# Kernel tuning notes

Measured on AMD Instinct MI355X. Metric: run time of the kernel, lower is better.

## Reference

```python
import jax, jax.numpy as jnp
import numpy as np

H = W = 512
P = H * W          # total superpixel member pixels
N_SP = 1024        # number of superpixels


def _conv(x, w, b):
    # x: [N,C,H,W], w: [O,I,3,3] -> [N,O,H,W], SAME padding
    y = jax.lax.conv_general_dilated(
        x, w, window_strides=(1, 1), padding='SAME',
        dimension_numbers=('NCHW', 'OIHW', 'NCHW'))
    return y + b[None, :, None, None]


def _embed(raw, w1, b1, w2, b2, w3, b3):
    h = jax.nn.relu(_conv(raw, w1, b1))
    h = jax.nn.relu(_conv(h, w2, b2))
    return _conv(h, w3, b3)  # [1, 10, H, W]


def setup_inputs() -> dict:
    key = jax.random.key(0)
    ks = jax.random.split(key, 6)
    raw = jax.random.normal(ks[0], (1, 1, H, W), dtype=jnp.float32)
    w1 = jax.random.normal(ks[1], (64, 1, 3, 3), dtype=jnp.float32) * 0.3
    b1 = jnp.zeros((64,), jnp.float32)
    w2 = jax.random.normal(ks[2], (64, 64, 3, 3), dtype=jnp.float32) * 0.05
    b2 = jnp.zeros((64,), jnp.float32)
    w3 = jax.random.normal(ks[3], (10, 64, 3, 3), dtype=jnp.float32) * 0.05
    b3 = jnp.zeros((10,), jnp.float32)
    pix_rc = jax.random.randint(ks[4], (P, 2), 0, H, dtype=jnp.int32)
    seg_ids = jax.random.randint(ks[5], (P,), 0, N_SP, dtype=jnp.int32)
    return {"raw": raw, "w1": w1, "b1": b1, "w2": w2, "b2": b2,
            "w3": w3, "b3": b3, "pix_rc": pix_rc, "seg_ids": seg_ids,
            "n_sp": N_SP}


def reference(raw, w1, b1, w2, b2, w3, b3, pix_rc, seg_ids, n_sp):
    feats = _embed(raw, w1, b1, w2, b2, w3, b3)  # [1, C, H, W]
    f = feats[0]                                  # [C, H, W]
    # gather per-pixel feature vectors: [P, C]
    vals = f[:, pix_rc[:, 0], pix_rc[:, 1]].T
    # scatter-mean over superpixels (= per-sp sum / mass)
    sums = jax.ops.segment_sum(vals, seg_ids, num_segments=n_sp)      # [n_sp, C]
    cnts = jax.ops.segment_sum(jnp.ones((vals.shape[0],), vals.dtype),
                               seg_ids, num_segments=n_sp)            # [n_sp]
    return sums / jnp.maximum(cnts, 1.0)[:, None]
```

## Files before the change

### kernel.cpp

```cpp
#include <hip/hip_runtime.h>

typedef __attribute__((ext_vector_type(8))) short short8;
typedef __attribute__((ext_vector_type(4))) float f32x4;

constexpr int H = 512, W = 512;
constexpr int P = H * W;
constexpr int NSP = 1024;
constexpr int SBLK = 512;
constexpr int FGRP = 16;

__device__ inline unsigned short f2bf(float f) {
  unsigned u = __builtin_bit_cast(unsigned, f);
  unsigned r = (u + 0x7fffu + ((u >> 16) & 1u)) >> 16;
  return (unsigned short)r;
}
__device__ inline float bflo(unsigned u) { return __builtin_bit_cast(float, u << 16); }
__device__ inline float bfhi(unsigned u) { return __builtin_bit_cast(float, u & 0xffff0000u); }

__device__ inline int xcd_swz(int b, int cpx) { return (b & 7) * cpx + (b >> 3); }

__global__ __launch_bounds__(256) void prep_k(const float* __restrict__ w2,
                                              const float* __restrict__ w3,
                                              unsigned short* __restrict__ wt2s,
                                              unsigned short* __restrict__ wt3s,
                                              unsigned short* __restrict__ zeros) {
  if (blockIdx.x == 0 && threadIdx.x < 128) zeros[threadIdx.x] = 0;
  int i = blockIdx.x * 256 + threadIdx.x;
  if (i < 36864) {
    int k = i >> 11;
    int t = (i >> 3) & 255;
    int e = i & 7;
    int r = t >> 2, sp = t & 3, s = sp ^ (r & 3);
    int tap = k >> 1, ic = (k & 1) * 32 + s * 8 + e;
    wt2s[i] = f2bf(w2[r * 576 + ic * 9 + tap]);
  } else if (i < 46080) {
    int j = i - 36864;
    int k = j >> 9;
    int t = (j >> 3) & 63;
    int e = j & 7;
    int r = t >> 2, sp = t & 3, s = sp ^ (r & 3);
    int tap = k >> 1, ic = (k & 1) * 32 + s * 8 + e;
    wt3s[j] = (r < 10) ? f2bf(w3[r * 576 + ic * 9 + tap]) : (unsigned short)0;
  }
}

__global__ __launch_bounds__(512) void conv2_k(const float* __restrict__ raw,
                                               const float* __restrict__ w1,
                                               const float* __restrict__ b1,
                                               const unsigned short* __restrict__ wts,
                                               const float* __restrict__ bias,
                                               unsigned short* __restrict__ ynhwc) {
  constexpr int WCS = 2048;
  __shared__ __align__(16) unsigned short acts[352 * 64];
  __shared__ __align__(16) unsigned short wbuf[3 * WCS];
  __shared__ float rawt[12 * 36];
  int tid = threadIdx.x;
  int lane = tid & 63, wave = tid >> 6;
  int logical = xcd_swz(blockIdx.x, 128);
  int tilex = logical & 15, tiley = logical >> 4;
  int c0 = tilex * 32, r0 = tiley * 8;

  if (tid < 256) {
#pragma unroll
    for (int k0 = 0; k0 < 2; ++k0) {
      const unsigned short* src = wts + (size_t)k0 * WCS + tid * 8;
      unsigned short* dstb = wbuf + k0 * WCS + wave * 512;
      __builtin_amdgcn_global_load_lds((const __attribute__((address_space(1))) void*)src,
                                       (__attribute__((address_space(3))) void*)dstb, 16, 0, 0);
    }
  }
  if (tid < 432) {
    int rr = tid / 36, cc = tid - rr * 36;
    int gr = r0 + rr - 2, gc = c0 + cc - 2;
    bool ok = ((unsigned)gr < 512u) && ((unsigned)gc < 512u);
    rawt[tid] = ok ? raw[gr * 512 + gc] : 0.f;
  }

  int q = lane >> 4, n = lane & 15;
  int og1 = wave & 3;
  short8 a1f;
  {
    short av[8];
#pragma unroll
    for (int e = 0; e < 8; ++e) av[e] = 0;
    int oc = og1 * 16 + n;
    if (q == 0) {
#pragma unroll
      for (int e = 0; e < 8; ++e) av[e] = (short)f2bf(w1[oc * 9 + e]);
    } else if (q == 1) {
      av[0] = (short)f2bf(w1[oc * 9 + 8]);
    }
    a1f = (short8){av[0], av[1], av[2], av[3], av[4], av[5], av[6], av[7]};
  }
  float bb1[4];
#pragma unroll
  for (int r2 = 0; r2 < 4; ++r2) bb1[r2] = b1[og1 * 16 + q * 4 + r2];
  __syncthreads();

  char* actw = (char*)acts;
  int tbase = (wave < 4) ? 0 : 11;
  for (int ti = 0; ti < 11; ++ti) {
    int t = tbase + ti;
    int px = t * 16 + n;
    bool okp = px < 340;
    int prow = px / 34, pcol = px - prow * 34;
    int prc = okp ? prow : 9;
    short bv[8];
#pragma unroll
    for (int e = 0; e < 8; ++e) bv[e] = 0;
    if (q == 0) {
#pragma unroll
      for (int e = 0; e < 8; ++e) {
        int dy = e / 3, dx = e - dy * 3;
        bv[e] = (short)f2bf(rawt[(prc + dy) * 36 + pcol + dx]);
      }
    } else if (q == 1) {
      bv[0] = (short)f2bf(rawt[(prc + 2) * 36 + pcol + 2]);
    }
    short8 b1f = (short8){bv[0], bv[1], bv[2], bv[3], bv[4], bv[5], bv[6], bv[7]};
    f32x4 d = __builtin_amdgcn_mfma_f32_16x16x32_bf16(a1f, b1f,
                                                       (f32x4){0.f, 0.f, 0.f, 0.f}, 0, 0, 0);
    int gr1 = r0 + prow - 1, gc1 = c0 + pcol - 1;
    bool ok1 = okp && ((unsigned)gr1 < 512u) && ((unsigned)gc1 < 512u);
    float o0 = ok1 ? fmaxf(d.x + bb1[0], 0.f) : 0.f;
    float o1 = ok1 ? fmaxf(d.y + bb1[1], 0.f) : 0.f;
    float o2 = ok1 ? fmaxf(d.z + bb1[2], 0.f) : 0.f;
    float o3 = ok1 ? fmaxf(d.w + bb1[3], 0.f) : 0.f;
    unsigned lo = (unsigned)f2bf(o0) | ((unsigned)f2bf(o1) << 16);
    unsigned hi = (unsigned)f2bf(o2) | ((unsigned)f2bf(o3) << 16);
    int wa = px * 128 + ((((og1 * 2 + (q >> 1)) ^ (px & 7)) << 4)) + ((q & 1) << 3);
    *reinterpret_cast<uint2*>(actw + wa) = make_uint2(lo, hi);
  }
  __syncthreads();

  f32x4 acc[4][2];
#pragma unroll
  for (int og = 0; og < 4; ++og)
#pragma unroll
    for (int g = 0; g < 2; ++g) acc[og][g] = (f32x4){0.f, 0.f, 0.f, 0.f};

  int plbase[2];
#pragma unroll
  for (int g = 0; g < 2; ++g) plbase[g] = wave * 34 + 16 * g + n;
  const char* actb = (const char*)acts;

#pragma unroll
  for (int k = 0; k < 18; ++k) {
    if (k == 17) {
      asm volatile("s_waitcnt vmcnt(0)" ::: "memory");
    } else {
      asm volatile("s_waitcnt vmcnt(1)" ::: "memory");
    }
    __builtin_amdgcn_sched_barrier(0);
    __builtin_amdgcn_s_barrier();
    __builtin_amdgcn_sched_barrier(0);
    if (k + 2 < 18 && tid < 256) {
      const unsigned short* src = wts + (size_t)(k + 2) * WCS + tid * 8;
      unsigned short* dstb = wbuf + ((k + 2) % 3) * WCS + wave * 512;
      __builtin_amdgcn_global_load_lds((const __attribute__((address_space(1))) void*)src,
                                       (__attribute__((address_space(3))) void*)dstb, 16, 0, 0);
    }
    const int tap = k >> 1, kc = k & 1;
    const int kyy = tap / 3, kxx = tap - kyy * 3;
    const char* wb = (const char*)(wbuf + (k % 3) * WCS);
    short8 af[4];
#pragma unroll
    for (int og = 0; og < 4; ++og) {
      int r = og * 16 + n;
      af[og] = *reinterpret_cast<const short8*>(wb + r * 64 + ((q ^ (r & 3)) * 16));
    }
#pragma unroll
    for (int g = 0; g < 2; ++g) {
      int pl = plbase[g] + kyy * 34 + kxx;
      int addr = pl * 128 + (((kc * 4 + q) ^ (pl & 7)) * 16);
      short8 bf = *reinterpret_cast<const short8*>(actb + addr);
#pragma unroll
      for (int og = 0; og < 4; ++og)
        acc[og][g] = __builtin_amdgcn_mfma_f32_16x16x32_bf16(af[og], bf, acc[og][g], 0, 0, 0);
    }
  }

  __syncthreads();
  char* ob = (char*)acts;
#pragma unroll
  for (int og = 0; og < 4; ++og) {
    float b0 = bias[og * 16 + q * 4 + 0], b1v = bias[og * 16 + q * 4 + 1];
    float b2 = bias[og * 16 + q * 4 + 2], b3 = bias[og * 16 + q * 4 + 3];
#pragma unroll
    for (int g = 0; g < 2; ++g) {
      int pl = wave * 32 + g * 16 + n;
      f32x4 v = acc[og][g];
      float o0 = fmaxf(v.x + b0, 0.f), o1 = fmaxf(v.y + b1v, 0.f);
      float o2 = fmaxf(v.z + b2, 0.f), o3 = fmaxf(v.w + b3, 0.f);
      unsigned lo = (unsigned)f2bf(o0) | ((unsigned)f2bf(o1) << 16);
      unsigned hi = (unsigned)f2bf(o2) | ((unsigned)f2bf(o3) << 16);
      int lslot = og * 2 + (q >> 1);
      int wa = pl * 128 + (((lslot ^ (pl & 7)) << 4)) + ((q & 1) << 3);
      *reinterpret_cast<uint2*>(ob + wa) = make_uint2(lo, hi);
    }
  }
  __syncthreads();
  char* yb = (char*)ynhwc;
#pragma unroll
  for (int it = 0; it < 4; ++it) {
    int c = it * 512 + tid;
    int pl = c >> 3, slot = c & 7;
    uint4 v = *reinterpret_cast<const uint4*>(ob + pl * 128 + ((slot ^ (pl & 7)) << 4));
    size_t gb = (((size_t)(r0 + (pl >> 5)) * 512) + c0 + (pl & 31)) * 128 + slot * 16;
    *reinterpret_cast<uint4*>(yb + gb) = v;
  }
}

__global__ __launch_bounds__(512) void conv3_k(const unsigned short* __restrict__ xin,
                                               const unsigned short* __restrict__ wts,
                                               const float* __restrict__ bias,
                                               unsigned short* __restrict__ feats,
                                               const unsigned short* __restrict__ zeros) {
  __shared__ __align__(16) unsigned short acts[352 * 64];
  __shared__ __align__(16) unsigned short wl[9216];
  int tid = threadIdx.x;
  int lane = tid & 63, wave = tid >> 6;
  int logical = xcd_swz(blockIdx.x, 128);
  int tilex = logical & 15, tiley = logical >> 4;
  int c0 = tilex * 32, r0 = tiley * 8;

  for (int wi = wave; wi < 18; wi += 8) {
    const unsigned short* src = wts + (size_t)wi * 512 + lane * 8;
    unsigned short* dstb = &wl[wi * 512];
    __builtin_amdgcn_global_load_lds((const __attribute__((address_space(1))) void*)src,
                                     (__attribute__((address_space(3))) void*)dstb, 16, 0, 0);
  }
  for (int wi = wave; wi < 44; wi += 8) {
    int cidx = wi * 64 + lane;
    int pix = cidx >> 3, slotp = cidx & 7;
    int prow = pix / 34, pcol = pix - prow * 34;
    int gr = r0 + prow - 1, gc = c0 + pcol - 1;
    int slot = slotp ^ (pix & 7);
    bool ok = (pix < 340) & ((unsigned)gr < 512u) & ((unsigned)gc < 512u);
    const unsigned short* src = ok ? (xin + (((size_t)(gr * 512 + gc)) << 6) + slot * 8) : zeros;
    unsigned short* dstb = &acts[wi * 512];
    __builtin_amdgcn_global_load_lds((const __attribute__((address_space(1))) void*)src,
                                     (__attribute__((address_space(3))) void*)dstb, 16, 0, 0);
  }
  __syncthreads();

  int q = lane >> 4, n = lane & 15;
  f32x4 acc[2];
#pragma unroll
  for (int g = 0; g < 2; ++g) acc[g] = (f32x4){0.f, 0.f, 0.f, 0.f};
  int plbase[2];
#pragma unroll
  for (int g = 0; g < 2; ++g) plbase[g] = wave * 34 + 16 * g + n;
  const char* actb = (const char*)acts;
  const char* wb0 = (const char*)wl;

#pragma unroll
  for (int k = 0; k < 18; ++k) {
    const int tap = k >> 1, kc = k & 1;
    const int kyy = tap / 3, kxx = tap - kyy * 3;
    short8 af = *reinterpret_cast<const short8*>(wb0 + k * 1024 + n * 64 + ((q ^ (n & 3)) * 16));
#pragma unroll
    for (int g = 0; g < 2; ++g) {
      int pl = plbase[g] + kyy * 34 + kxx;
      int addr = pl * 128 + (((kc * 4 + q) ^ (pl & 7)) * 16);
      short8 bf = *reinterpret_cast<const short8*>(actb + addr);
      acc[g] = __builtin_amdgcn_mfma_f32_16x16x32_bf16(af, bf, acc[g], 0, 0, 0);
    }
  }

  __syncthreads();
  char* ob = (char*)acts;
  float bb[4];
#pragma unroll
  for (int r2 = 0; r2 < 4; ++r2) {
    int oc = q * 4 + r2;
    bb[r2] = (oc < 10) ? bias[oc] : 0.f;
  }
#pragma unroll
  for (int g = 0; g < 2; ++g) {
    int pl = wave * 32 + g * 16 + n;
    f32x4 v = acc[g];
    float o0 = v.x + bb[0], o1 = v.y + bb[1], o2 = v.z + bb[2], o3 = v.w + bb[3];
    if (q < 2) {
      unsigned u0 = (unsigned)f2bf(o0) | ((unsigned)f2bf(o1) << 16);
      unsigned u1 = (unsigned)f2bf(o2) | ((unsigned)f2bf(o3) << 16);
      *reinterpret_cast<uint2*>(ob + pl * 24 + q * 8) = make_uint2(u0, u1);
    } else if (q == 2) {
      *reinterpret_cast<unsigned*>(ob + pl * 24 + 16) =
          (unsigned)f2bf(o0) | ((unsigned)f2bf(o1) << 16);
    }
  }
  __syncthreads();
  char* fb = (char*)feats;
#pragma unroll
  for (int it = 0; it < 3; ++it) {
    int c = it * 512 + tid;
    if (c < 1280) {
      int row = c / 160, wb = c - row * 160;
      int byte = wb * 4;
      int px = byte / 20, off = byte - px * 20;
      unsigned v = *reinterpret_cast<const unsigned*>(ob + (row * 32 + px) * 24 + off);
      size_t gbyte = (((size_t)(r0 + row) * 512) + c0) * 20 + (size_t)byte;
      *reinterpret_cast<unsigned*>(fb + gbyte) = v;
    }
  }
}

__global__ __launch_bounds__(512) void scatter_k(const unsigned short* __restrict__ feats,
                                                 const int* __restrict__ pix_rc,
                                                 const int* __restrict__ seg,
                                                 float* __restrict__ partials) {
  __shared__ float ls[NSP * 10];
  __shared__ float lc[NSP];
  int tid = threadIdx.x;
  for (int i = tid; i < NSP * 10; i += 512) ls[i] = 0.f;
  for (int i = tid; i < NSP; i += 512) lc[i] = 0.f;
  __syncthreads();

  constexpr int PER = P / SBLK;
  int p0 = blockIdx.x * PER;
  for (int p = p0 + tid; p < p0 + PER; p += 512) {
    int r = pix_rc[2 * p], c = pix_rc[2 * p + 1];
    int s = seg[p];
    size_t gpix = (size_t)r * 512 + c;
    const char* fp = (const char*)feats + gpix * 20;
    uint4 a = *reinterpret_cast<const uint4*>(fp);
    unsigned e = *reinterpret_cast<const unsigned*>(fp + 16);
    float v[10];
    v[0] = bflo(a.x); v[1] = bfhi(a.x);
    v[2] = bflo(a.y); v[3] = bfhi(a.y);
    v[4] = bflo(a.z); v[5] = bfhi(a.z);
    v[6] = bflo(a.w); v[7] = bfhi(a.w);
    v[8] = bflo(e);   v[9] = bfhi(e);
#pragma unroll
    for (int ch = 0; ch < 10; ++ch) atomicAdd(&ls[s * 10 + ch], v[ch]);
    atomicAdd(&lc[s], 1.f);
  }
  __syncthreads();

  float* outp = partials + (size_t)blockIdx.x * (NSP * 11);
  for (int i = tid; i < NSP * 10; i += 512) outp[i] = ls[i];
  for (int i = tid; i < NSP; i += 512) outp[NSP * 10 + i] = lc[i];
}

__global__ __launch_bounds__(256) void finA_k(const float* __restrict__ partials,
                                              float* __restrict__ partials2) {
  int g = blockIdx.x / 44;
  int e = (blockIdx.x - g * 44) * 256 + threadIdx.x;
  const float* base = partials + (size_t)(g * 32) * (NSP * 11) + e;
  float s = 0.f;
#pragma unroll 8
  for (int k = 0; k < 32; ++k) s += base[(size_t)k * (NSP * 11)];
  partials2[(size_t)g * (NSP * 11) + e] = s;
}

__global__ __launch_bounds__(256) void finB_k(const float* __restrict__ partials2,
                                              float* __restrict__ out) {
  int i = blockIdx.x * 256 + threadIdx.x;
  if (i >= NSP * 10) return;
  int sp = i / 10;
  float s = 0.f, cnt = 0.f;
#pragma unroll
  for (int g = 0; g < FGRP; ++g) {
    const float* pp = partials2 + (size_t)g * (NSP * 11);
    s += pp[i];
    cnt += pp[NSP * 10 + sp];
  }
  out[i] = s / fmaxf(cnt, 1.f);
}

extern "C" void kernel_launch(void* const* d_in, const int* in_sizes, int n_in,
                              void* d_out, int out_size, void* d_ws, size_t ws_size,
                              hipStream_t stream) {
  const float* raw = (const float*)d_in[0];
  const float* w1  = (const float*)d_in[1];
  const float* b1  = (const float*)d_in[2];
  const float* w2  = (const float*)d_in[3];
  const float* b2  = (const float*)d_in[4];
  const float* w3  = (const float*)d_in[5];
  const float* b3  = (const float*)d_in[6];
  const int* pix_rc = (const int*)d_in[7];
  const int* seg    = (const int*)d_in[8];
  float* out = (float*)d_out;

  char* ws = (char*)d_ws;
  unsigned short* h2   = (unsigned short*)(ws + 33554432);
  unsigned short* feats = (unsigned short*)(ws + 67108864);
  unsigned short* wt2s = (unsigned short*)(ws + 72351744);
  unsigned short* wt3s = (unsigned short*)(ws + 72425472);
  unsigned short* zeros = (unsigned short*)(ws + 72443904);
  float* partials  = (float*)(ws + 0);
  float* partials2 = (float*)(ws + 23068672);

  prep_k<<<180, 256, 0, stream>>>(w2, w3, wt2s, wt3s, zeros);
  conv2_k<<<1024, 512, 0, stream>>>(raw, w1, b1, wt2s, b2, h2);
  conv3_k<<<1024, 512, 0, stream>>>(h2, wt3s, b3, feats, zeros);
  scatter_k<<<SBLK, 512, 0, stream>>>(feats, pix_rc, seg, partials);
  finA_k<<<FGRP * 44, 256, 0, stream>>>(partials, partials2);
  finB_k<<<40, 256, 0, stream>>>(partials2, out);
}
```

Measured before the change: 83.66 us.

## Fuse conv2 and conv3 into one kernel with halo recompute

Result: no change. 85.21 us (+1.8%).

```diff
diff --git a/kernel.cpp b/kernel.cpp
--- a/kernel.cpp
+++ b/kernel.cpp
@@ -22,9 +22,7 @@
 __global__ __launch_bounds__(256) void prep_k(const float* __restrict__ w2,
                                               const float* __restrict__ w3,
                                               unsigned short* __restrict__ wt2s,
-                                              unsigned short* __restrict__ wt3s,
-                                              unsigned short* __restrict__ zeros) {
-  if (blockIdx.x == 0 && threadIdx.x < 128) zeros[threadIdx.x] = 0;
+                                              unsigned short* __restrict__ wt3s) {
   int i = blockIdx.x * 256 + threadIdx.x;
   if (i < 36864) {
     int k = i >> 11;
@@ -44,16 +42,18 @@
   }
 }
 
-__global__ __launch_bounds__(512) void conv2_k(const float* __restrict__ raw,
-                                               const float* __restrict__ w1,
-                                               const float* __restrict__ b1,
-                                               const unsigned short* __restrict__ wts,
-                                               const float* __restrict__ bias,
-                                               unsigned short* __restrict__ ynhwc) {
+__global__ __launch_bounds__(512, 4) void conv123_k(const float* __restrict__ raw,
+                                                    const float* __restrict__ w1,
+                                                    const float* __restrict__ b1,
+                                                    const unsigned short* __restrict__ wts2,
+                                                    const float* __restrict__ b2,
+                                                    const unsigned short* __restrict__ wts3,
+                                                    const float* __restrict__ b3,
+                                                    unsigned short* __restrict__ feats) {
   constexpr int WCS = 2048;
-  __shared__ __align__(16) unsigned short acts[352 * 64];
+  __shared__ __align__(16) unsigned short acts[448 * 64];
   __shared__ __align__(16) unsigned short wbuf[3 * WCS];
-  __shared__ float rawt[12 * 36];
+  __shared__ float rawt[14 * 38];
   int tid = threadIdx.x;
   int lane = tid & 63, wave = tid >> 6;
   int logical = xcd_swz(blockIdx.x, 128);
@@ -63,17 +63,17 @@
   if (tid < 256) {
 #pragma unroll
     for (int k0 = 0; k0 < 2; ++k0) {
-      const unsigned short* src = wts + (size_t)k0 * WCS + tid * 8;
+      const unsigned short* src = wts2 + (size_t)k0 * WCS + tid * 8;
       unsigned short* dstb = wbuf + k0 * WCS + wave * 512;
       __builtin_amdgcn_global_load_lds((const __attribute__((address_space(1))) void*)src,
                                        (__attribute__((address_space(3))) void*)dstb, 16, 0, 0);
     }
   }
-  if (tid < 432) {
-    int rr = tid / 36, cc = tid - rr * 36;
-    int gr = r0 + rr - 2, gc = c0 + cc - 2;
+  for (int i = tid; i < 532; i += 512) {
+    int rr = i / 38, cc = i - rr * 38;
+    int gr = r0 + rr - 3, gc = c0 + cc - 3;
     bool ok = ((unsigned)gr < 512u) && ((unsigned)gc < 512u);
-    rawt[tid] = ok ? raw[gr * 512 + gc] : 0.f;
+    rawt[i] = ok ? raw[gr * 512 + gc] : 0.f;
   }
 
   int q = lane >> 4, n = lane & 15;
@@ -98,13 +98,12 @@
   __syncthreads();
 
   char* actw = (char*)acts;
-  int tbase = (wave < 4) ? 0 : 11;
-  for (int ti = 0; ti < 11; ++ti) {
-    int t = tbase + ti;
+  int hhalf = wave >> 2;
+  for (int i1 = 0; i1 < 14; ++i1) {
+    int t = 2 * i1 + hhalf;
+    if (t >= 27) break;
     int px = t * 16 + n;
-    bool okp = px < 340;
-    int prow = px / 34, pcol = px - prow * 34;
-    int prc = okp ? prow : 9;
+    int py = px / 36, pxc = px - py * 36;
     short bv[8];
 #pragma unroll
     for (int e = 0; e < 8; ++e) bv[e] = 0;
@@ -112,16 +111,16 @@
 #pragma unroll
       for (int e = 0; e < 8; ++e) {
         int dy = e / 3, dx = e - dy * 3;
-        bv[e] = (short)f2bf(rawt[(prc + dy) * 36 + pcol + dx]);
+        bv[e] = (short)f2bf(rawt[(py + dy) * 38 + pxc + dx]);
       }
     } else if (q == 1) {
-      bv[0] = (short)f2bf(rawt[(prc + 2) * 36 + pcol + 2]);
+      bv[0] = (short)f2bf(rawt[(py + 2) * 38 + pxc + 2]);
     }
     short8 b1f = (short8){bv[0], bv[1], bv[2], bv[3], bv[4], bv[5], bv[6], bv[7]};
     f32x4 d = __builtin_amdgcn_mfma_f32_16x16x32_bf16(a1f, b1f,
                                                        (f32x4){0.f, 0.f, 0.f, 0.f}, 0, 0, 0);
-    int gr1 = r0 + prow - 1, gc1 = c0 + pcol - 1;
-    bool ok1 = okp && ((unsigned)gr1 < 512u) && ((unsigned)gc1 < 512u);
+    int gr1 = r0 + py - 2, gc1 = c0 + pxc - 2;
+    bool ok1 = ((unsigned)gr1 < 512u) && ((unsigned)gc1 < 512u);
     float o0 = ok1 ? fmaxf(d.x + bb1[0], 0.f) : 0.f;
     float o1 = ok1 ? fmaxf(d.y + bb1[1], 0.f) : 0.f;
     float o2 = ok1 ? fmaxf(d.z + bb1[2], 0.f) : 0.f;
@@ -133,15 +132,11 @@
   }
   __syncthreads();
 
-  f32x4 acc[4][2];
+  f32x4 acc[4][3];
 #pragma unroll
   for (int og = 0; og < 4; ++og)
 #pragma unroll
-    for (int g = 0; g < 2; ++g) acc[og][g] = (f32x4){0.f, 0.f, 0.f, 0.f};
-
-  int plbase[2];
-#pragma unroll
-  for (int g = 0; g < 2; ++g) plbase[g] = wave * 34 + 16 * g + n;
+    for (int g = 0; g < 3; ++g) acc[og][g] = (f32x4){0.f, 0.f, 0.f, 0.f};
   const char* actb = (const char*)acts;
 
 #pragma unroll
@@ -155,7 +150,7 @@
     __builtin_amdgcn_s_barrier();
     __builtin_amdgcn_sched_barrier(0);
     if (k + 2 < 18 && tid < 256) {
-      const unsigned short* src = wts + (size_t)(k + 2) * WCS + tid * 8;
+      const unsigned short* src = wts2 + (size_t)(k + 2) * WCS + tid * 8;
       unsigned short* dstb = wbuf + ((k + 2) % 3) * WCS + wave * 512;
       __builtin_amdgcn_global_load_lds((const __attribute__((address_space(1))) void*)src,
                                        (__attribute__((address_space(3))) void*)dstb, 16, 0, 0);
@@ -170,117 +165,97 @@
       af[og] = *reinterpret_cast<const short8*>(wb + r * 64 + ((q ^ (r & 3)) * 16));
     }
 #pragma unroll
+    for (int g = 0; g < 3; ++g) {
+      int t2 = wave + 8 * g;
+      if (t2 < 23) {
+        int pl = t2 * 16 + n + kyy * 36 + kxx;
+        int addr = pl * 128 + (((kc * 4 + q) ^ (pl & 7)) * 16);
+        short8 bf = *reinterpret_cast<const short8*>(actb + addr);
+#pragma unroll
+        for (int og = 0; og < 4; ++og)
+          acc[og][g] = __builtin_amdgcn_mfma_f32_16x16x32_bf16(af[og], bf, acc[og][g], 0, 0, 0);
+      }
+    }
+  }
+  __syncthreads();
+
+  if (tid < 64) {
+#pragma unroll
+    for (int k0 = 0; k0 < 2; ++k0) {
+      const unsigned short* src = wts3 + (size_t)k0 * 512 + lane * 8;
+      unsigned short* dstb = &wbuf[k0 * 512];
+      __builtin_amdgcn_global_load_lds((const __attribute__((address_space(1))) void*)src,
+                                       (__attribute__((address_space(3))) void*)dstb, 16, 0, 0);
+    }
+  }
+#pragma unroll
+  for (int g = 0; g < 3; ++g) {
+    int t2 = wave + 8 * g;
+    if (t2 < 23) {
+      int px2 = t2 * 16 + n;
+#pragma unroll
+      for (int og = 0; og < 4; ++og) {
+        f32x4 v = acc[og][g];
+        float o0 = fmaxf(v.x + b2[og * 16 + q * 4 + 0], 0.f);
+        float o1 = fmaxf(v.y + b2[og * 16 + q * 4 + 1], 0.f);
+        float o2 = fmaxf(v.z + b2[og * 16 + q * 4 + 2], 0.f);
+        float o3 = fmaxf(v.w + b2[og * 16 + q * 4 + 3], 0.f);
+        unsigned lo = (unsigned)f2bf(o0) | ((unsigned)f2bf(o1) << 16);
+        unsigned hi = (unsigned)f2bf(o2) | ((unsigned)f2bf(o3) << 16);
+        int lslot = og * 2 + (q >> 1);
+        int wa = px2 * 128 + (((lslot ^ (px2 & 7)) << 4)) + ((q & 1) << 3);
+        *reinterpret_cast<uint2*>(actw + wa) = make_uint2(lo, hi);
+      }
+    }
+  }
+  __syncthreads();
+
+  f32x4 acc3[2];
+#pragma unroll
+  for (int g = 0; g < 2; ++g) acc3[g] = (f32x4){0.f, 0.f, 0.f, 0.f};
+  const char* wb3 = (const char*)wbuf;
+
+#pragma unroll
+  for (int k = 0; k < 18; ++k) {
+    if (k == 17) {
+      asm volatile("s_waitcnt vmcnt(0)" ::: "memory");
+    } else {
+      asm volatile("s_waitcnt vmcnt(1)" ::: "memory");
+    }
+    __builtin_amdgcn_sched_barrier(0);
+    __builtin_amdgcn_s_barrier();
+    __builtin_amdgcn_sched_barrier(0);
+    if (k + 2 < 18 && tid < 64) {
+      const unsigned short* src = wts3 + (size_t)(k + 2) * 512 + lane * 8;
+      unsigned short* dstb = &wbuf[((k + 2) % 3) * 512];
+      __builtin_amdgcn_global_load_lds((const __attribute__((address_space(1))) void*)src,
+                                       (__attribute__((address_space(3))) void*)dstb, 16, 0, 0);
+    }
+    const int tap = k >> 1, kc = k & 1;
+    const int kyy = tap / 3, kxx = tap - kyy * 3;
+    short8 af = *reinterpret_cast<const short8*>(wb3 + (k % 3) * 1024 + n * 64 + ((q ^ (n & 3)) * 16));
+#pragma unroll
     for (int g = 0; g < 2; ++g) {
-      int pl = plbase[g] + kyy * 34 + kxx;
+      int pl = wave * 36 + g * 16 + n + kyy * 36 + kxx;
       int addr = pl * 128 + (((kc * 4 + q) ^ (pl & 7)) * 16);
       short8 bf = *reinterpret_cast<const short8*>(actb + addr);
-#pragma unroll
-      for (int og = 0; og < 4; ++og)
-        acc[og][g] = __builtin_amdgcn_mfma_f32_16x16x32_bf16(af[og], bf, acc[og][g], 0, 0, 0);
+      acc3[g] = __builtin_amdgcn_mfma_f32_16x16x32_bf16(af, bf, acc3[g], 0, 0, 0);
     }
   }
 
   __syncthreads();
   char* ob = (char*)acts;
-#pragma unroll
-  for (int og = 0; og < 4; ++og) {
-    float b0 = bias[og * 16 + q * 4 + 0], b1v = bias[og * 16 + q * 4 + 1];
-    float b2 = bias[og * 16 + q * 4 + 2], b3 = bias[og * 16 + q * 4 + 3];
-#pragma unroll
-    for (int g = 0; g < 2; ++g) {
-      int pl = wave * 32 + g * 16 + n;
-      f32x4 v = acc[og][g];
-      float o0 = fmaxf(v.x + b0, 0.f), o1 = fmaxf(v.y + b1v, 0.f);
-      float o2 = fmaxf(v.z + b2, 0.f), o3 = fmaxf(v.w + b3, 0.f);
-      unsigned lo = (unsigned)f2bf(o0) | ((unsigned)f2bf(o1) << 16);
-      unsigned hi = (unsigned)f2bf(o2) | ((unsigned)f2bf(o3) << 16);
-      int lslot = og * 2 + (q >> 1);
-      int wa = pl * 128 + (((lslot ^ (pl & 7)) << 4)) + ((q & 1) << 3);
-      *reinterpret_cast<uint2*>(ob + wa) = make_uint2(lo, hi);
-    }
-  }
-  __syncthreads();
-  char* yb = (char*)ynhwc;
-#pragma unroll
-  for (int it = 0; it < 4; ++it) {
-    int c = it * 512 + tid;
-    int pl = c >> 3, slot = c & 7;
-    uint4 v = *reinterpret_cast<const uint4*>(ob + pl * 128 + ((slot ^ (pl & 7)) << 4));
-    size_t gb = (((size_t)(r0 + (pl >> 5)) * 512) + c0 + (pl & 31)) * 128 + slot * 16;
-    *reinterpret_cast<uint4*>(yb + gb) = v;
-  }
-}
-
-__global__ __launch_bounds__(512) void conv3_k(const unsigned short* __restrict__ xin,
-                                               const unsigned short* __restrict__ wts,
-                                               const float* __restrict__ bias,
-                                               unsigned short* __restrict__ feats,
-                                               const unsigned short* __restrict__ zeros) {
-  __shared__ __align__(16) unsigned short acts[352 * 64];
-  __shared__ __align__(16) unsigned short wl[9216];
-  int tid = threadIdx.x;
-  int lane = tid & 63, wave = tid >> 6;
-  int logical = xcd_swz(blockIdx.x, 128);
-  int tilex = logical & 15, tiley = logical >> 4;
-  int c0 = tilex * 32, r0 = tiley * 8;
-
-  for (int wi = wave; wi < 18; wi += 8) {
-    const unsigned short* src = wts + (size_t)wi * 512 + lane * 8;
-    unsigned short* dstb = &wl[wi * 512];
-    __builtin_amdgcn_global_load_lds((const __attribute__((address_space(1))) void*)src,
-                                     (__attribute__((address_space(3))) void*)dstb, 16, 0, 0);
-  }
-  for (int wi = wave; wi < 44; wi += 8) {
-    int cidx = wi * 64 + lane;
-    int pix = cidx >> 3, slotp = cidx & 7;
-    int prow = pix / 34, pcol = pix - prow * 34;
-    int gr = r0 + prow - 1, gc = c0 + pcol - 1;
-    int slot = slotp ^ (pix & 7);
-    bool ok = (pix < 340) & ((unsigned)gr < 512u) & ((unsigned)gc < 512u);
-    const unsigned short* src = ok ? (xin + (((size_t)(gr * 512 + gc)) << 6) + slot * 8) : zeros;
-    unsigned short* dstb = &acts[wi * 512];
-    __builtin_amdgcn_global_load_lds((const __attribute__((address_space(1))) void*)src,
-                                     (__attribute__((address_space(3))) void*)dstb, 16, 0, 0);
-  }
-  __syncthreads();
-
-  int q = lane >> 4, n = lane & 15;
-  f32x4 acc[2];
-#pragma unroll
-  for (int g = 0; g < 2; ++g) acc[g] = (f32x4){0.f, 0.f, 0.f, 0.f};
-  int plbase[2];
-#pragma unroll
-  for (int g = 0; g < 2; ++g) plbase[g] = wave * 34 + 16 * g + n;
-  const char* actb = (const char*)acts;
-  const char* wb0 = (const char*)wl;
-
-#pragma unroll
-  for (int k = 0; k < 18; ++k) {
-    const int tap = k >> 1, kc = k & 1;
-    const int kyy = tap / 3, kxx = tap - kyy * 3;
-    short8 af = *reinterpret_cast<const short8*>(wb0 + k * 1024 + n * 64 + ((q ^ (n & 3)) * 16));
-#pragma unroll
-    for (int g = 0; g < 2; ++g) {
-      int pl = plbase[g] + kyy * 34 + kxx;
-      int addr = pl * 128 + (((kc * 4 + q) ^ (pl & 7)) * 16);
-      short8 bf = *reinterpret_cast<const short8*>(actb + addr);
-      acc[g] = __builtin_amdgcn_mfma_f32_16x16x32_bf16(af, bf, acc[g], 0, 0, 0);
-    }
-  }
-
-  __syncthreads();
-  char* ob = (char*)acts;
-  float bb[4];
+  float bb3[4];
 #pragma unroll
   for (int r2 = 0; r2 < 4; ++r2) {
     int oc = q * 4 + r2;
-    bb[r2] = (oc < 10) ? bias[oc] : 0.f;
+    bb3[r2] = (oc < 10) ? b3[oc] : 0.f;
   }
 #pragma unroll
   for (int g = 0; g < 2; ++g) {
     int pl = wave * 32 + g * 16 + n;
-    f32x4 v = acc[g];
-    float o0 = v.x + bb[0], o1 = v.y + bb[1], o2 = v.z + bb[2], o3 = v.w + bb[3];
+    f32x4 v = acc3[g];
+    float o0 = v.x + bb3[0], o1 = v.y + bb3[1], o2 = v.z + bb3[2], o3 = v.w + bb3[3];
     if (q < 2) {
       unsigned u0 = (unsigned)f2bf(o0) | ((unsigned)f2bf(o1) << 16);
       unsigned u1 = (unsigned)f2bf(o2) | ((unsigned)f2bf(o3) << 16);
@@ -384,17 +359,14 @@
   float* out = (float*)d_out;
 
   char* ws = (char*)d_ws;
-  unsigned short* h2   = (unsigned short*)(ws + 33554432);
-  unsigned short* feats = (unsigned short*)(ws + 67108864);
-  unsigned short* wt2s = (unsigned short*)(ws + 72351744);
-  unsigned short* wt3s = (unsigned short*)(ws + 72425472);
-  unsigned short* zeros = (unsigned short*)(ws + 72443904);
   float* partials  = (float*)(ws + 0);
   float* partials2 = (float*)(ws + 23068672);
-
-  prep_k<<<180, 256, 0, stream>>>(w2, w3, wt2s, wt3s, zeros);
-  conv2_k<<<1024, 512, 0, stream>>>(raw, w1, b1, wt2s, b2, h2);
-  conv3_k<<<1024, 512, 0, stream>>>(h2, wt3s, b3, feats, zeros);
+  unsigned short* feats = (unsigned short*)(ws + 25165824);
+  unsigned short* wt2s = (unsigned short*)(ws + 30408704);
+  unsigned short* wt3s = (unsigned short*)(ws + 30482432);
+
+  prep_k<<<180, 256, 0, stream>>>(w2, w3, wt2s, wt3s);
+  conv123_k<<<1024, 512, 0, stream>>>(raw, w1, b1, wt2s, b2, wt3s, b3, feats);
   scatter_k<<<SBLK, 512, 0, stream>>>(feats, pix_rc, seg, partials);
   finA_k<<<FGRP * 44, 256, 0, stream>>>(partials, partials2);
   finB_k<<<40, 256, 0, stream>>>(partials2, out);
```
